# Kernel optimization log

Measured on AMD Instinct MI355X. Metric: run time of the kernel, lower is better.

## Reference

```python
import jax, jax.numpy as jnp
import numpy as np

N_NODES = 4_000_000
N_GRAPHS = 4096  # B; fixed for jit (torch derives it from batch.max()+1)
D_FEAT = 8
NUM_CLASSES = 10


def setup_inputs() -> dict:
    key = jax.random.key(0)
    k1, k2, k3, k4, k5 = jax.random.split(key, 5)
    x = jax.random.normal(k1, (N_NODES, D_FEAT), dtype=jnp.float32)
    # sorted segment ids; with ~977 nodes/graph expected, empty segments are vanishingly unlikely
    batch_ids = jnp.sort(jax.random.randint(k2, (N_NODES,), 0, N_GRAPHS, dtype=jnp.int64))
    input_ids = jax.random.randint(k3, (N_GRAPHS, 128), 0, 30522, dtype=jnp.int64)
    attention_mask = jnp.ones((N_GRAPHS, 128), dtype=jnp.int64)
    W = jax.random.normal(k4, (NUM_CLASSES, D_FEAT), dtype=jnp.float32) * (1.0 / np.sqrt(D_FEAT))
    b = jax.random.normal(k5, (NUM_CLASSES,), dtype=jnp.float32) * 0.01
    return {"x": x, "batch_ids": batch_ids, "input_ids": input_ids,
            "attention_mask": attention_mask, "W": W, "b": b}


def reference(x, batch_ids, input_ids, attention_mask, W, b):
    # Segment-mean pooling: replaces the O(B) python loop of masked means
    # with a single-pass scatter-add. input_ids / attention_mask are unused
    # by the original forward (kept for signature fidelity).
    sums = jax.ops.segment_sum(x, batch_ids, num_segments=N_GRAPHS)          # [B, 8]
    counts = jax.ops.segment_sum(jnp.ones((x.shape[0],), x.dtype), batch_ids,
                                 num_segments=N_GRAPHS)                      # [B]
    pooled = sums / counts[:, None]                                          # [B, 8]
    logits = pooled @ W.T + b                                                # [B, 10]
    return logits
```

## Files before the change

kernel.cpp:

```cpp
#include <hip/hip_runtime.h>

constexpr int N_NODES  = 4000000;
constexpr int N_GRAPHS = 4096;
constexpr int D_FEAT   = 8;
constexpr int N_CLS    = 10;
constexpr int CHUNK    = 512;
constexpr int NCH      = (N_NODES + CHUNK - 1) / CHUNK;
constexpr int ACC_F32  = N_GRAPHS * D_FEAT + N_GRAPHS;

typedef float f32x4 __attribute__((ext_vector_type(4)));
typedef int   i32x4 __attribute__((ext_vector_type(4)));


__global__ __launch_bounds__(256) void pool_seg(
    const f32x4* __restrict__ xf,
    const i32x4* __restrict__ ids4,
    const int*   __restrict__ ids,
    float*       __restrict__ sums,
    float*       __restrict__ cnts)
{
    int w = blockIdx.x * 4 + (threadIdx.x >> 6);
    if (w >= NCH) return;
    int lane = threadIdx.x & 63;
    int c0 = w * CHUNK;
    int c1 = min(c0 + CHUNK, N_NODES);

    int base = c0 + lane * 8;
    i32x4 v0, v1;
    if (base + 8 <= N_NODES) {
        v0 = ids4[base >> 2];
        v1 = ids4[(base >> 2) + 1];
    } else {
        int last = ids[N_NODES - 1];
        v0 = (i32x4)(last);
        v1 = (i32x4)(last);
    }
    int gcur = __shfl(v0.x, 0);
    int p = c0;

    while (true) {
        unsigned m8 = 0;
        m8 |= (v0.x != gcur && base + 0 > p) ? 1u   : 0u;
        m8 |= (v0.y != gcur && base + 1 > p) ? 2u   : 0u;
        m8 |= (v0.z != gcur && base + 2 > p) ? 4u   : 0u;
        m8 |= (v0.w != gcur && base + 3 > p) ? 8u   : 0u;
        m8 |= (v1.x != gcur && base + 4 > p) ? 16u  : 0u;
        m8 |= (v1.y != gcur && base + 5 > p) ? 32u  : 0u;
        m8 |= (v1.z != gcur && base + 6 > p) ? 64u  : 0u;
        m8 |= (v1.w != gcur && base + 7 > p) ? 128u : 0u;

        int j0   = __builtin_ctz(m8 | 0x100u);
        int cpos = base + j0;
        int cid  = j0 < 4 ? (j0 < 2 ? (j0 == 0 ? v0.x : v0.y)
                                    : (j0 == 2 ? v0.z : v0.w))
                          : (j0 < 6 ? (j0 == 4 ? v1.x : v1.y)
                                    : (j0 == 6 ? v1.z : v1.w));
        unsigned long long ball = __ballot(m8 != 0);
        int pend = c1, gnext = 0;
        if (ball != 0ull) {
            int fl = __builtin_ctzll(ball);
            pend  = __shfl(cpos, fl);
            gnext = __shfl(cid,  fl);
        }

        f32x4 a0 = (f32x4)(0.f), a1 = (f32x4)(0.f),
              a2 = (f32x4)(0.f), a3 = (f32x4)(0.f);
        int i    = 2 * p + lane;
        int endf = 2 * pend;
        int full = (endf - 2 * p) >> 8;
        for (int it = 0; it < full; ++it, i += 256) {
            a0 += xf[i];
            a1 += xf[i +  64];
            a2 += xf[i + 128];
            a3 += xf[i + 192];
        }
        for (; i < endf; i += 64) a0 += xf[i];
        f32x4 acc = (a0 + a1) + (a2 + a3);

        #pragma unroll
        for (int off = 32; off >= 2; off >>= 1) {
            acc.x += __shfl_xor(acc.x, off);
            acc.y += __shfl_xor(acc.y, off);
            acc.z += __shfl_xor(acc.z, off);
            acc.w += __shfl_xor(acc.w, off);
        }
        if (lane < 2) {
            float* s = sums + (size_t)gcur * D_FEAT + lane * 4;
            atomicAdd(s + 0, acc.x);
            atomicAdd(s + 1, acc.y);
            atomicAdd(s + 2, acc.z);
            atomicAdd(s + 3, acc.w);
        }
        if (lane == 0)
            atomicAdd(cnts + gcur, (float)(pend - p));

        if (pend >= c1) break;
        p = pend; gcur = gnext;
    }
}

__global__ __launch_bounds__(256) void finalize(
    const float* __restrict__ sums, const float* __restrict__ cnts,
    const float* __restrict__ W, const float* __restrict__ bias,
    float* __restrict__ out)
{
    int idx = blockIdx.x * blockDim.x + threadIdx.x;
    if (idx >= N_GRAPHS * N_CLS) return;
    int g = idx / N_CLS;
    int c = idx % N_CLS;
    float inv = 1.0f / cnts[g];
    const float* s = sums + (size_t)g * D_FEAT;
    const float* w = W + (size_t)c * D_FEAT;
    float a = bias[c];
    #pragma unroll
    for (int k = 0; k < D_FEAT; ++k)
        a += (s[k] * inv) * w[k];
    out[idx] = a;
}

extern "C" void kernel_launch(void* const* d_in, const int* in_sizes, int n_in,
                              void* d_out, int out_size, void* d_ws, size_t ws_size,
                              hipStream_t stream) {
    const float* x   = (const float*)d_in[0];
    const int*   ids = (const int*)d_in[1];
    const float* W   = (const float*)d_in[4];
    const float* b   = (const float*)d_in[5];
    float*       out = (float*)d_out;

    float* sums = (float*)d_ws;
    float* cnts = sums + (size_t)N_GRAPHS * D_FEAT;

    hipMemsetAsync(d_ws, 0, (size_t)ACC_F32 * sizeof(float), stream);

    int pool_blocks = (NCH + 3) / 4;
    pool_seg<<<pool_blocks, 256, 0, stream>>>(
        (const f32x4*)x, (const i32x4*)ids, ids, sums, cnts);

    finalize<<<(N_GRAPHS * N_CLS + 255) / 256, 256, 0, stream>>>(
        sums, cnts, W, b, out);
}
```

Baseline: 35.47 us.

## Replace per-segment loop with single-pass two-accumulator chunk reduction

Each wave now counts segment boundaries in its 512-node chunk up front with a neighbour shuffle and a popcount reduction. When a chunk holds at most one boundary, which is the common case at about 977 nodes per graph, it streams the whole chunk once into two accumulator sets split at the boundary and flushes each with a wave reduction and atomics. This removes the data-dependent while loop, the repeated ballot and shuffle work, and the shorter serial sub-loops that ran whenever a segment was split. Chunks with several boundaries fall back to per-node atomics, which are slow but should be rare. The common path needs more registers and adds a select per element in the boundary iteration.

```diff
diff --git a/kernel.cpp b/kernel.cpp
--- a/kernel.cpp
+++ b/kernel.cpp
@@ -11,13 +11,40 @@
 typedef float f32x4 __attribute__((ext_vector_type(4)));
 typedef int   i32x4 __attribute__((ext_vector_type(4)));
 
+__device__ __forceinline__ int idat(const i32x4& v0, const i32x4& v1, int j) {
+    switch (j) {
+        case 0: return v0.x; case 1: return v0.y;
+        case 2: return v0.z; case 3: return v0.w;
+        case 4: return v1.x; case 5: return v1.y;
+        case 6: return v1.z; default: return v1.w;
+    }
+}
+
+__device__ __forceinline__ void wave_flush(
+    f32x4 acc, int lane, int g, float cnt,
+    float* __restrict__ sums, float* __restrict__ cnts)
+{
+    #pragma unroll
+    for (int off = 32; off >= 2; off >>= 1) {
+        acc.x += __shfl_xor(acc.x, off);
+        acc.y += __shfl_xor(acc.y, off);
+        acc.z += __shfl_xor(acc.z, off);
+        acc.w += __shfl_xor(acc.w, off);
+    }
+    if (lane < 2) {
+        float* s = sums + (size_t)g * D_FEAT + lane * 4;
+        atomicAdd(s + 0, acc.x);
+        atomicAdd(s + 1, acc.y);
+        atomicAdd(s + 2, acc.z);
+        atomicAdd(s + 3, acc.w);
+    }
+    if (lane == 0) atomicAdd(cnts + g, cnt);
+}
 
 __global__ __launch_bounds__(256) void pool_seg(
-    const f32x4* __restrict__ xf,
-    const i32x4* __restrict__ ids4,
-    const int*   __restrict__ ids,
-    float*       __restrict__ sums,
-    float*       __restrict__ cnts)
+    const f32x4* __restrict__ xf, const float* __restrict__ x,
+    const i32x4* __restrict__ ids4, const int* __restrict__ ids,
+    float* __restrict__ sums, float* __restrict__ cnts)
 {
     int w = blockIdx.x * 4 + (threadIdx.x >> 6);
     if (w >= NCH) return;
@@ -31,71 +58,76 @@
         v0 = ids4[base >> 2];
         v1 = ids4[(base >> 2) + 1];
     } else {
-        int last = ids[N_NODES - 1];
-        v0 = (i32x4)(last);
-        v1 = (i32x4)(last);
+        i32x4 l = (i32x4)(ids[N_NODES - 1]);
+        v0 = l; v1 = l;
     }
     int gcur = __shfl(v0.x, 0);
-    int p = c0;
 
-    while (true) {
-        unsigned m8 = 0;
-        m8 |= (v0.x != gcur && base + 0 > p) ? 1u   : 0u;
-        m8 |= (v0.y != gcur && base + 1 > p) ? 2u   : 0u;
-        m8 |= (v0.z != gcur && base + 2 > p) ? 4u   : 0u;
-        m8 |= (v0.w != gcur && base + 3 > p) ? 8u   : 0u;
-        m8 |= (v1.x != gcur && base + 4 > p) ? 16u  : 0u;
-        m8 |= (v1.y != gcur && base + 5 > p) ? 32u  : 0u;
-        m8 |= (v1.z != gcur && base + 6 > p) ? 64u  : 0u;
-        m8 |= (v1.w != gcur && base + 7 > p) ? 128u : 0u;
+    int pl = __shfl(v1.w, (lane == 0) ? 0 : (lane - 1));
+    int pv = (lane == 0) ? v0.x : pl;
+    unsigned m8 = 0;
+    m8 |= (v0.x != pv)   ? 1u   : 0u;
+    m8 |= (v0.y != v0.x) ? 2u   : 0u;
+    m8 |= (v0.z != v0.y) ? 4u   : 0u;
+    m8 |= (v0.w != v0.z) ? 8u   : 0u;
+    m8 |= (v1.x != v0.w) ? 16u  : 0u;
+    m8 |= (v1.y != v1.x) ? 32u  : 0u;
+    m8 |= (v1.z != v1.y) ? 64u  : 0u;
+    m8 |= (v1.w != v1.z) ? 128u : 0u;
 
-        int j0   = __builtin_ctz(m8 | 0x100u);
-        int cpos = base + j0;
-        int cid  = j0 < 4 ? (j0 < 2 ? (j0 == 0 ? v0.x : v0.y)
-                                    : (j0 == 2 ? v0.z : v0.w))
-                          : (j0 < 6 ? (j0 == 4 ? v1.x : v1.y)
-                                    : (j0 == 6 ? v1.z : v1.w));
-        unsigned long long ball = __ballot(m8 != 0);
-        int pend = c1, gnext = 0;
-        if (ball != 0ull) {
-            int fl = __builtin_ctzll(ball);
-            pend  = __shfl(cpos, fl);
-            gnext = __shfl(cid,  fl);
+    int tot = __popc(m8);
+    #pragma unroll
+    for (int off = 32; off; off >>= 1) tot += __shfl_xor(tot, off);
+
+    if (tot <= 1) {
+        int bnd = c1, gnext = 0;
+        if (tot == 1) {
+            int j   = __builtin_ctz(m8 | 0x100u);
+            int pos = base + j;
+            int idj = idat(v0, v1, j);
+            unsigned long long ball = __ballot(m8 != 0);
+            int fl = (int)__builtin_ctzll(ball);
+            bnd   = __shfl(pos, fl);
+            gnext = __shfl(idj, fl);
         }
+        int bf = 2 * bnd;
+        f32x4 z = (f32x4)(0.f);
+        f32x4 aA0=z, aA1=z, aA2=z, aA3=z;
+        f32x4 aB0=z, aB1=z, aB2=z, aB3=z;
 
-        f32x4 a0 = (f32x4)(0.f), a1 = (f32x4)(0.f),
-              a2 = (f32x4)(0.f), a3 = (f32x4)(0.f);
-        int i    = 2 * p + lane;
-        int endf = 2 * pend;
-        int full = (endf - 2 * p) >> 8;
-        for (int it = 0; it < full; ++it, i += 256) {
-            a0 += xf[i];
-            a1 += xf[i +  64];
-            a2 += xf[i + 128];
-            a3 += xf[i + 192];
+        int u    = 2 * c0;
+        int uend = u + 2 * (c1 - c0);
+        for (; u < uend; u += 256) {
+            int i0 = u + lane;
+            f32x4 x0 = xf[i0], x1 = xf[i0+64], x2 = xf[i0+128], x3 = xf[i0+192];
+            if (u + 256 <= bf) {
+                aA0 += x0; aA1 += x1; aA2 += x2; aA3 += x3;
+            } else if (u >= bf) {
+                aB0 += x0; aB1 += x1; aB2 += x2; aB3 += x3;
+            } else {
+                aA0 += (i0       < bf) ? x0 : z;  aB0 += (i0       < bf) ? z : x0;
+                aA1 += (i0 +  64 < bf) ? x1 : z;  aB1 += (i0 +  64 < bf) ? z : x1;
+                aA2 += (i0 + 128 < bf) ? x2 : z;  aB2 += (i0 + 128 < bf) ? z : x2;
+                aA3 += (i0 + 192 < bf) ? x3 : z;  aB3 += (i0 + 192 < bf) ? z : x3;
+            }
         }
-        for (; i < endf; i += 64) a0 += xf[i];
-        f32x4 acc = (a0 + a1) + (a2 + a3);
-
-        #pragma unroll
-        for (int off = 32; off >= 2; off >>= 1) {
-            acc.x += __shfl_xor(acc.x, off);
-            acc.y += __shfl_xor(acc.y, off);
-            acc.z += __shfl_xor(acc.z, off);
-            acc.w += __shfl_xor(acc.w, off);
+        wave_flush((aA0 + aA1) + (aA2 + aA3), lane, gcur,
+                   (float)(bnd - c0), sums, cnts);
+        if (bnd < c1)
+            wave_flush((aB0 + aB1) + (aB2 + aB3), lane, gnext,
+                       (float)(c1 - bnd), sums, cnts);
+    } else {
+        for (int j = 0; j < 8; ++j) {
+            int n = base + j;
+            if (n < c1) {
+                int g = idat(v0, v1, j);
+                #pragma unroll
+                for (int k = 0; k < D_FEAT; ++k)
+                    atomicAdd(&sums[(size_t)g * D_FEAT + k],
+                              x[(size_t)n * D_FEAT + k]);
+                atomicAdd(&cnts[g], 1.0f);
+            }
         }
-        if (lane < 2) {
-            float* s = sums + (size_t)gcur * D_FEAT + lane * 4;
-            atomicAdd(s + 0, acc.x);
-            atomicAdd(s + 1, acc.y);
-            atomicAdd(s + 2, acc.z);
-            atomicAdd(s + 3, acc.w);
-        }
-        if (lane == 0)
-            atomicAdd(cnts + gcur, (float)(pend - p));
-
-        if (pend >= c1) break;
-        p = pend; gcur = gnext;
     }
 }
 
@@ -134,7 +166,7 @@
 
     int pool_blocks = (NCH + 3) / 4;
     pool_seg<<<pool_blocks, 256, 0, stream>>>(
-        (const f32x4*)x, (const i32x4*)ids, ids, sums, cnts);
+        (const f32x4*)x, x, (const i32x4*)ids, ids, sums, cnts);
 
     finalize<<<(N_GRAPHS * N_CLS + 255) / 256, 256, 0, stream>>>(
         sums, cnts, W, b, out);
```

Result: no change. 35.03 us (-1.2%).
